# Kernel tuning notes

Measured on AMD Instinct MI355X. Metric: run time of the kernel, lower is better.

Reference implementation:

```python
import jax, jax.numpy as jnp
import numpy as np

DIM = 2048
NUM_HEADS = 16
NUM_KV_HEADS = 4
HEAD_DIM = DIM // NUM_HEADS  # 128
ROPE_BASE = 10000.0
TRAIN_SEQ_LEN = 1024
EPS = 1.1920929e-07  # torch.finfo(float32).eps, used by F.rms_norm default


def _rope_tables(seq_len, dtype=jnp.float32):
    rd = HEAD_DIM  # rope_dims defaults to full head_dim
    if seq_len > TRAIN_SEQ_LEN:
        s = seq_len / TRAIN_SEQ_LEN
        base = ROPE_BASE * s ** (rd / (rd - 2))
    else:
        base = ROPE_BASE
    inv_freq = 1.0 / base ** (jnp.arange(0, rd, 2, dtype=jnp.float32) / rd)
    t = jnp.arange(seq_len, dtype=jnp.float32)
    freqs = jnp.outer(t, inv_freq)  # [S, rd//2]
    cos = jnp.cos(freqs)[None, :, None, :].astype(dtype)  # [1,S,1,rd//2]
    sin = jnp.sin(freqs)[None, :, None, :].astype(dtype)
    return cos, sin


def _rms_norm(x):
    var = jnp.mean(jnp.square(x), axis=-1, keepdims=True)
    return x * jax.lax.rsqrt(var + EPS)


def _apply_rotary(x, cos, sin):
    h = x.shape[-1] // 2
    x1, x2 = x[..., :h], x[..., h:]
    return jnp.concatenate((x1 * cos + x2 * sin, -x1 * sin + x2 * cos), axis=-1)


def setup_inputs() -> dict:
    key = jax.random.key(0)
    ks = jax.random.split(key, 6)
    B, S = 2, 2048
    kv_dim = NUM_KV_HEADS * HEAD_DIM
    x = jax.random.normal(ks[0], (B, S, DIM), dtype=jnp.float32)
    Wq = jax.random.normal(ks[1], (DIM, DIM), dtype=jnp.float32) * 0.02
    Wk = jax.random.normal(ks[2], (kv_dim, DIM), dtype=jnp.float32) * 0.02
    Wv = jax.random.normal(ks[3], (kv_dim, DIM), dtype=jnp.float32) * 0.02
    Wo = jax.random.normal(ks[4], (DIM, DIM), dtype=jnp.float32) * 0.02
    q_gain = jnp.full((NUM_HEADS,), 1.0, dtype=jnp.float32)
    return {"x": x, "Wq": Wq, "Wk": Wk, "Wv": Wv, "Wo": Wo, "q_gain": q_gain}


def reference(x, Wq, Wk, Wv, Wo, q_gain):
    B, S, D = x.shape
    H, Hkv, Dh = NUM_HEADS, NUM_KV_HEADS, HEAD_DIM
    # QKV projections (CastedLinear, no bias)
    q = (x @ Wq.T).reshape(B, S, H, Dh)
    k = (x @ Wk.T).reshape(B, S, Hkv, Dh)
    v = (x @ Wv.T).reshape(B, S, Hkv, Dh)
    # RMSNorm over head_dim (no learned weight)
    q = _rms_norm(q)
    k = _rms_norm(k)
    # RoPE (full head_dim, NTK-scaled since S > train_seq_len)
    cos, sin = _rope_tables(S, q.dtype)
    q = _apply_rotary(q, cos, sin)
    k = _apply_rotary(k, cos, sin)
    # per-head gain on q
    q = q * q_gain.astype(q.dtype)[None, None, :, None]
    # GQA: repeat_interleave kv heads
    reps = H // Hkv
    k = jnp.repeat(k, reps, axis=2)  # [B,S,H,Dh]
    v = jnp.repeat(v, reps, axis=2)
    # causal attention
    scale = 1.0 / jnp.sqrt(jnp.asarray(Dh, dtype=q.dtype))
    scores = jnp.einsum('bqhd,bkhd->bhqk', q, k) * scale  # [B,H,S,S]
    causal = jnp.tril(jnp.ones((S, S), dtype=bool))
    scores = jnp.where(causal[None, None], scores, jnp.finfo(scores.dtype).min)
    attn = jax.nn.softmax(scores, axis=-1)
    y = jnp.einsum('bhqk,bkhd->bqhd', attn, v)  # [B,S,H,Dh]
    return y.reshape(B, S, D) @ Wo.T
```

## Files before the change

kernel.cpp:

```cpp
#include <hip/hip_runtime.h>

#define DIMSZ 2048
#define NHEAD 16
#define NKV 4
#define HD 128
#define QKVD 3072
#define SEQ 2048
#define NTOK 4096

typedef __attribute__((ext_vector_type(8))) short short8;
typedef __attribute__((ext_vector_type(4))) float f32x4;
typedef unsigned short u16;

__device__ __forceinline__ u16 f2bf(float x) {
  union { float f; unsigned u; } v; v.f = x;
  unsigned r = v.u + 0x7fffu + ((v.u >> 16) & 1u);
  return (u16)(r >> 16);
}
__device__ __forceinline__ unsigned pack_bf2(float a, float b) {
  unsigned ua = __float_as_uint(a) + 0x8000u;
  unsigned ub = __float_as_uint(b) + 0x8000u;
  return __builtin_amdgcn_perm(ub, ua, 0x07060302);
}

__device__ __forceinline__ void gl_lds16(const void* g, void* l) {
  __builtin_amdgcn_global_load_lds(
      (const __attribute__((address_space(1))) void*)g,
      (__attribute__((address_space(3))) void*)l, 16, 0, 0);
}

template <int N> __device__ __forceinline__ void vmw() {
  asm volatile("s_waitcnt vmcnt(%0)" :: "n"(N) : "memory");
}
__device__ __forceinline__ void barsb() {
  __builtin_amdgcn_s_barrier();
  __builtin_amdgcn_sched_barrier(0);
}

__global__ __launch_bounds__(256)
void castAll(const float* __restrict__ x,  const float* __restrict__ Wq,
             const float* __restrict__ Wk, const float* __restrict__ Wv,
             const float* __restrict__ Wo, u16* __restrict__ xb,
             u16* __restrict__ Wqkvb, u16* __restrict__ Wob) {
  int i = blockIdx.x * 256 + threadIdx.x;
  int f = i * 4;
  const float* src; u16* dst; int off;
  if (f < 8388608)       { src = x;  dst = xb;    off = f; }
  else if (f < 12582912) { src = Wq; dst = Wqkvb; off = f - 8388608; }
  else if (f < 13631488) { src = Wk; dst = Wqkvb + 4194304; off = f - 12582912; }
  else if (f < 14680064) { src = Wv; dst = Wqkvb + 5242880; off = f - 13631488; }
  else                   { src = Wo; dst = Wob;   off = f - 14680064; }
  float4 v = *(const float4*)(src + off);
  ushort4 o;
  o.x = f2bf(v.x); o.y = f2bf(v.y); o.z = f2bf(v.z); o.w = f2bf(v.w);
  *(ushort4*)(dst + off) = o;
}

template <int NCT, bool F32OUT>
__global__ __launch_bounds__(512, 2)
void gemmX(const u16* __restrict__ A, const u16* __restrict__ W,
           void* __restrict__ Cv, int M, int N, int K) {
  __shared__ __align__(16) u16 As[2][256][64];
  __shared__ __align__(16) u16 Bs[2][NCT * 64][64];
  const int tid = threadIdx.x;
  const int l = tid & 63;
  const int w = tid >> 6;
  const int r = l & 15, q = l >> 4;
  const int wm = (w >> 2) * 128;
  const int wn = (w & 3) * (NCT * 16);

  const int nx  = N / (NCT * 64);
  const int cpx = gridDim.x >> 3;
  const int lid = (blockIdx.x & 7) * cpx + (blockIdx.x >> 3);
  const int m0 = (lid / nx) << 8;
  const int n0 = (lid % nx) * (NCT * 64);

  const int scol = ((l & 7) ^ (l >> 3)) << 3;
  const u16* Asrc = A + (long)(m0 + w * 8 + (l >> 3)) * K + scol;
  const u16* Bsrc = W + (long)(n0 + w * 8 + (l >> 3)) * K + scol;

  auto stA = [&](int d, int u, int kt) {
    gl_lds16(Asrc + (long)(u * 64) * K + kt * 64, &As[d][u * 64 + w * 8][0]);
  };
  auto stB = [&](int d, int u, int kt) {
    gl_lds16(Bsrc + (long)(u * 64) * K + kt * 64, &Bs[d][u * 64 + w * 8][0]);
  };
  auto lda = [&](int d, int rt, int ks) -> short8 {
    return *(const short8*)&As[d][wm + rt * 16 + r][(((ks << 2) | q) ^ (r & 7)) << 3];
  };
  auto ldb = [&](int d, int ct, int ks) -> short8 {
    return *(const short8*)&Bs[d][wn + ct * 16 + r][(((ks << 2) | q) ^ (r & 7)) << 3];
  };

  f32x4 acc[8][NCT] = {};
  short8 a[4][2];
  short8 bE[NCT][2];
  short8 bO[NCT][2];

#define QUAD(i_, AB, BR)                                                      \
  _Pragma("unroll") for (int ks_ = 0; ks_ < 2; ++ks_)                         \
  _Pragma("unroll") for (int c_ = 0; c_ < NCT; ++c_)                          \
    acc[(AB) + (i_)][c_] = __builtin_amdgcn_mfma_f32_16x16x32_bf16(           \
        a[i_][ks_], BR[c_][ks_], acc[(AB) + (i_)][c_], 0, 0, 0);

#pragma unroll
  for (int u = 0; u < NCT; ++u) stB(0, u, 0);
  stA(0, 0, 0); stA(0, 1, 0); stA(0, 2, 0); stA(0, 3, 0);
#pragma unroll
  for (int u = 0; u < NCT; ++u) stB(1, u, 1);
  stA(1, 0, 1); stA(1, 2, 1);
  vmw<NCT + 2>();
  barsb();
#pragma unroll
  for (int i = 0; i < 4; ++i) { a[i][0] = lda(0, i, 0); a[i][1] = lda(0, i, 1); }
#pragma unroll
  for (int c = 0; c < NCT; ++c) { bE[c][0] = ldb(0, c, 0); bE[c][1] = ldb(0, c, 1); }

  const int niter = K >> 7;
  for (int it = 0; it < niter; ++it) {
    const int kt1 = 2 * it + 1, kt2 = 2 * it + 2, kt3 = 2 * it + 3;
    const bool more = (it + 1 < niter);

    stA(1, 1, kt1); stA(1, 3, kt1);
    __builtin_amdgcn_s_setprio(1);
#pragma unroll
    for (int i_ = 0; i_ < 4; ++i_) {
      QUAD(i_, 0, bE);
      a[i_][0] = lda(0, 4 + i_, 0); a[i_][1] = lda(0, 4 + i_, 1);
    }
    __builtin_amdgcn_s_setprio(0);
    vmw<2>();
    barsb();

    if (more) {
#pragma unroll
      for (int u = 0; u < NCT; ++u) stB(0, u, kt2);
      stA(0, 0, kt2); stA(0, 2, kt2);
    }
    __builtin_amdgcn_s_setprio(1);
#pragma unroll
    for (int i_ = 0; i_ < 4; ++i_) {
      QUAD(i_, 4, bE);
      a[i_][0] = lda(1, i_, 0); a[i_][1] = lda(1, i_, 1);
      if (i_ == 0) {
#pragma unroll
        for (int c = 0; c < NCT; ++c) { bO[c][0] = ldb(1, c, 0); bO[c][1] = ldb(1, c, 1); }
      }
    }
    __builtin_amdgcn_s_setprio(0);
    if (more) vmw<NCT + 2>(); else vmw<0>();
    barsb();

    if (more) { stA(0, 1, kt2); stA(0, 3, kt2); }
    __builtin_amdgcn_s_setprio(1);
#pragma unroll
    for (int i_ = 0; i_ < 4; ++i_) {
      QUAD(i_, 0, bO);
      a[i_][0] = lda(1, 4 + i_, 0); a[i_][1] = lda(1, 4 + i_, 1);
    }
    __builtin_amdgcn_s_setprio(0);
    if (more) vmw<2>();
    barsb();

    if (more) {
#pragma unroll
      for (int u = 0; u < NCT; ++u) stB(1, u, kt3);
      stA(1, 0, kt3); stA(1, 2, kt3);
    }
    __builtin_amdgcn_s_setprio(1);
#pragma unroll
    for (int i_ = 0; i_ < 4; ++i_) {
      QUAD(i_, 4, bO);
      if (more) {
        a[i_][0] = lda(0, i_, 0); a[i_][1] = lda(0, i_, 1);
        if (i_ == 0) {
#pragma unroll
          for (int c = 0; c < NCT; ++c) { bE[c][0] = ldb(0, c, 0); bE[c][1] = ldb(0, c, 1); }
        }
      }
    }
    __builtin_amdgcn_s_setprio(0);
    if (more) vmw<NCT + 2>();
    barsb();
  }
#undef QUAD

#pragma unroll
  for (int i = 0; i < 8; ++i)
#pragma unroll
    for (int j = 0; j < NCT; ++j) {
      int row = m0 + wm + i * 16 + q * 4;
      int col = n0 + wn + j * 16 + r;
#pragma unroll
      for (int t = 0; t < 4; ++t) {
        if (F32OUT)
          ((float*)Cv)[(long)(row + t) * N + col] = acc[i][j][t];
        else
          ((u16*)Cv)[(long)(row + t) * N + col] = f2bf(acc[i][j][t]);
      }
    }
}

__global__ __launch_bounds__(256)
void prep(u16* __restrict__ qkv, const float* __restrict__ gain, float qsc,
          u16* __restrict__ vt) {
  if (blockIdx.x < 20480) {
    int gid  = blockIdx.x * 4 + (threadIdx.x >> 6);
    int lane = threadIdx.x & 63;
    int token = gid / 20;
    int idx   = gid % 20;
    int s     = token & (SEQ - 1);
    bool isq  = idx < 16;
    int off   = isq ? idx * HD : 2048 + (idx - 16) * HD;
    float psc = isq ? qsc * gain[idx & 15] : 1.0f;
    u16* p = qkv + (long)token * QKVD + off;
    union { unsigned u; float f; } c1, c2;
    c1.u = ((unsigned)p[lane]) << 16;
    c2.u = ((unsigned)p[lane + 64]) << 16;
    float x1 = c1.f, x2 = c2.f;
    float ss = x1 * x1 + x2 * x2;
#pragma unroll
    for (int d = 1; d < 64; d <<= 1) ss += __shfl_xor(ss, d);
    float rn = rsqrtf(ss * (1.0f / 128.0f) + 1.1920929e-07f) * psc;
    float lb = log2f(10000.0f) + 128.0f / 126.0f;
    float inv_freq = exp2f(-(float)lane * (lb * (1.0f / 64.0f)));
    float ang = (float)s * inv_freq;
    float sn, cs;
    sincosf(ang, &sn, &cs);
    p[lane]      = f2bf((x1 * cs + x2 * sn) * rn);
    p[lane + 64] = f2bf((-x1 * sn + x2 * cs) * rn);
  } else {
    __shared__ u16 T[128 * 72];
    int bid = blockIdx.x - 20480;
    const int k0 = (bid & 31) * 64, hkv = (bid >> 5) & 3, b = bid >> 7;
    const u16* vb = qkv + 2560;
    const int t = threadIdx.x;
    const int key = t & 63, dh0 = (t >> 6) * 32;
#pragma unroll
    for (int c = 0; c < 4; c++) {
      uint4 vv = *(const uint4*)&vb[(long)(b * SEQ + k0 + key) * QKVD + hkv * HD + dh0 + c * 8];
      u16 tmp[8];
      *(uint4*)tmp = vv;
#pragma unroll
      for (int e = 0; e < 8; e++) T[(dh0 + c * 8 + e) * 72 + key] = tmp[e];
    }
    __syncthreads();
    const int dh = t >> 1, half = t & 1;
#pragma unroll
    for (int c = 0; c < 4; c++) {
      uint4 ov = *(const uint4*)&T[dh * 72 + half * 32 + c * 8];
      *(uint4*)&vt[((long)(b * NKV + hkv) * HD + dh) * SEQ + k0 + half * 32 + c * 8] = ov;
    }
  }
}

__global__ __launch_bounds__(256, 4)
void fattn(const u16* __restrict__ qb, const u16* __restrict__ kb,
           const u16* __restrict__ vtg, u16* __restrict__ yb) {
  __shared__ u16 Ks[64 * 128];
  __shared__ u16 Vt[128 * 64];
  __shared__ u16 Ps[64 * 64];
  const int tid  = threadIdx.x;
  const int lane = tid & 63;
  const int w    = tid >> 6;
  const int r = lane & 15, q = lane >> 4;
  const int qt = 31 - (blockIdx.x >> 5);
  const int hb = blockIdx.x & 31;
  const int h  = hb >> 1;
  const int b  = hb & 1;
  const int q0 = qt * 64;
  const int hkv = h >> 2;

  long koff[4], voff[4];
  u16 *kdst[4], *vdst[4];
#pragma unroll
  for (int c = 0; c < 4; c++) {
    int gr = w * 16 + c * 4 + (lane >> 4);
    int s  = lane & 15;
    int kj = (s & 8) | ((s ^ gr) & 7);
    koff[c] = (long)gr * QKVD + hkv * HD + kj * 8;
    kdst[c] = Ks + (w * 16 + c * 4) * 128;
    int dh = (w * 4 + c) * 8 + (lane >> 3);
    int vs = lane & 7;
    int vj = (vs ^ dh) & 7;
    voff[c] = (long)dh * SEQ + vj * 8;
    vdst[c] = Vt + (w * 4 + c) * 8 * 64;
  }
  const u16* vbase = vtg + (long)(b * NKV + hkv) * HD * SEQ;

  short8 qf[4];
#pragma unroll
  for (int ks = 0; ks < 4; ks++)
    qf[ks] = *(const short8*)&qb[(long)(b * SEQ + q0 + w * 16 + r) * QKVD +
                                 h * HD + ks * 32 + q * 8];

  f32x4 oacc[8] = {};
  float l_i = 0.f;
  const int maskbase = q * 4 - w * 16 - r;
  const int psx = (r & 7) << 1;

  for (int k0 = 0; k0 <= q0; k0 += 64) {
    __syncthreads();
    const u16* kb_t = kb + (long)(b * SEQ + k0) * QKVD;
    const u16* vb_t = vbase + k0;
#pragma unroll
    for (int c = 0; c < 4; c++) {
      gl_lds16(kb_t + koff[c], kdst[c]);
      gl_lds16(vb_t + voff[c], vdst[c]);
    }
    __syncthreads();

    const bool maskit = (k0 == q0);

    f32x4 st[4] = {};
#pragma unroll
    for (int jt = 0; jt < 4; jt++)
#pragma unroll
      for (int ks = 0; ks < 4; ks++) {
        int row = jt * 16 + r;
        int j = ks * 4 + q;
        int p = (j & 8) | ((j ^ row) & 7);
        short8 kf = *(const short8*)&Ks[row * 128 + p * 8];
        st[jt] = __builtin_amdgcn_mfma_f32_16x16x32_bf16(kf, qf[ks], st[jt], 0, 0, 0);
      }

    if (maskit) {
#pragma unroll
      for (int jt = 0; jt < 4; jt++)
#pragma unroll
        for (int t = 0; t < 4; t++)
          if (jt * 16 + maskbase + t > 0) st[jt][t] = -3e38f;
    }

#pragma unroll
    for (int jt = 0; jt < 4; jt++) {
#pragma unroll
      for (int t = 0; t < 4; t++) {
        float p = exp2f(st[jt][t]);
        st[jt][t] = p;
      }
      l_i += (st[jt][0] + st[jt][1]) + (st[jt][2] + st[jt][3]);
      uint2 pk;
      pk.x = pack_bf2(st[jt][0], st[jt][1]);
      pk.y = pack_bf2(st[jt][2], st[jt][3]);
      *(uint2*)&Ps[(w * 16 + r) * 64 + ((jt * 4 + q) ^ psx) * 4] = pk;
    }
    asm volatile("s_waitcnt lgkmcnt(0)" ::: "memory");

#pragma unroll
    for (int ks = 0; ks < 2; ks++) {
      short8 pf = *(const short8*)&Ps[(w * 16 + r) * 64 + ((ks * 8 + q * 2) ^ psx) * 4];
#pragma unroll
      for (int n = 0; n < 8; n++) {
        int row = n * 16 + r;
        int j = ks * 4 + q;
        int p = (j ^ row) & 7;
        short8 vf = *(const short8*)&Vt[row * 64 + p * 8];
        oacc[n] = __builtin_amdgcn_mfma_f32_16x16x32_bf16(pf, vf, oacc[n], 0, 0, 0);
      }
    }
  }

  l_i += __shfl_xor(l_i, 16);
  l_i += __shfl_xor(l_i, 32);
  float lb4[4];
#pragma unroll
  for (int t = 0; t < 4; t++) lb4[t] = 1.0f / __shfl(l_i, q * 4 + t);
#pragma unroll
  for (int n = 0; n < 8; n++)
#pragma unroll
    for (int t = 0; t < 4; t++) {
      int row = q0 + w * 16 + q * 4 + t;
      int col = n * 16 + r;
      yb[(long)(b * SEQ + row) * DIMSZ + h * HD + col] = f2bf(oacc[n][t] * lb4[t]);
    }
}

extern "C" void kernel_launch(void* const* d_in, const int* in_sizes, int n_in,
                              void* d_out, int out_size, void* d_ws, size_t ws_size,
                              hipStream_t stream) {
  const float* x  = (const float*)d_in[0];
  const float* Wq = (const float*)d_in[1];
  const float* Wk = (const float*)d_in[2];
  const float* Wv = (const float*)d_in[3];
  const float* Wo = (const float*)d_in[4];
  const float* qg = (const float*)d_in[5];
  float* out = (float*)d_out;

  const long MB = 1024 * 1024;
  char* ws = (char*)d_ws;
  u16* xb    = (u16*)(ws + 0 * MB);
  u16* ybuf  = (u16*)(ws + 0 * MB);
  u16* Wqkvb = (u16*)(ws + 16 * MB);
  u16* Wob   = (u16*)(ws + 28 * MB);
  u16* qkv   = (u16*)(ws + 36 * MB);
  u16* vtg   = (u16*)(ws + 60 * MB);

  castAll<<<18432, 256, 0, stream>>>(x, Wq, Wk, Wv, Wo, xb, Wqkvb, Wob);

  gemmX<3, false><<<256, 512, 0, stream>>>(xb, Wqkvb, qkv, NTOK, QKVD, DIMSZ);

  const float qsc = 0.08838834764831845f * 1.44269504088896f;
  prep<<<20736, 256, 0, stream>>>(qkv, qg, qsc, vtg);

  fattn<<<1024, 256, 0, stream>>>(qkv, qkv + 2048, vtg, ybuf);

  gemmX<2, true><<<256, 512, 0, stream>>>(ybuf, Wob, out, NTOK, DIMSZ, DIMSZ);
}
```

Before: 296.6 us.

## Rewrite flash attention with 32x32 MFMA, 128-query tiles and register P

Restructures the attention kernel to use 32x32x16 bf16 MFMA with 128-row query tiles per block (32 rows per wave), halving the grid. The softmax probabilities stay in registers and are rearranged with v_permlane32_swap for the PV MFMA, so the Ps LDS buffer and its round trip go away. The block ordering is changed to pair long and short causal tiles, aimed at load balancing and at reusing each K/V tile across more queries. Occupancy drops to 2 blocks per CU, and there is one extra diagonal K tile iteration per block.

New measurement: 303.7 us. +2.4%, slower.

```diff
diff --git a/kernel.cpp b/kernel.cpp
--- a/kernel.cpp
+++ b/kernel.cpp
@@ -10,6 +10,7 @@
 
 typedef __attribute__((ext_vector_type(8))) short short8;
 typedef __attribute__((ext_vector_type(4))) float f32x4;
+typedef __attribute__((ext_vector_type(16))) float f32x16;
 typedef unsigned short u16;
 
 __device__ __forceinline__ u16 f2bf(float x) {
@@ -254,52 +255,66 @@
   }
 }
 
-__global__ __launch_bounds__(256, 4)
+__global__ __launch_bounds__(256, 2)
 void fattn(const u16* __restrict__ qb, const u16* __restrict__ kb,
            const u16* __restrict__ vtg, u16* __restrict__ yb) {
   __shared__ u16 Ks[64 * 128];
   __shared__ u16 Vt[128 * 64];
-  __shared__ u16 Ps[64 * 64];
-  const int tid  = threadIdx.x;
-  const int lane = tid & 63;
-  const int w    = tid >> 6;
-  const int r = lane & 15, q = lane >> 4;
-  const int qt = 31 - (blockIdx.x >> 5);
-  const int hb = blockIdx.x & 31;
-  const int h  = hb >> 1;
-  const int b  = hb & 1;
-  const int q0 = qt * 64;
+  const int tid = threadIdx.x;
+  const int l   = tid & 63;
+  const int w   = tid >> 6;
+  const int lh  = l >> 5;
+  const int l31 = l & 31;
+  const int bq  = blockIdx.x >> 5;
+  const int qt  = (blockIdx.x & 256) ? (bq - 8) : (15 - bq);
+  const int hb  = blockIdx.x & 31;
+  const int h   = hb >> 1;
+  const int b   = hb & 1;
+  const int q0  = qt * 128;
   const int hkv = h >> 2;
-
-  long koff[4], voff[4];
+  const int qrow = q0 + w * 32 + l31;
+
+  int koff[4], voff[4];
   u16 *kdst[4], *vdst[4];
 #pragma unroll
   for (int c = 0; c < 4; c++) {
-    int gr = w * 16 + c * 4 + (lane >> 4);
-    int s  = lane & 15;
-    int kj = (s & 8) | ((s ^ gr) & 7);
-    koff[c] = (long)gr * QKVD + hkv * HD + kj * 8;
+    int gr = w * 16 + c * 4 + (l >> 4);
+    int s  = l & 15;
+    int kj = s ^ (gr & 15);
+    koff[c] = gr * QKVD + hkv * HD + kj * 8;
     kdst[c] = Ks + (w * 16 + c * 4) * 128;
-    int dh = (w * 4 + c) * 8 + (lane >> 3);
-    int vs = lane & 7;
-    int vj = (vs ^ dh) & 7;
-    voff[c] = (long)dh * SEQ + vj * 8;
-    vdst[c] = Vt + (w * 4 + c) * 8 * 64;
+    int dh = w * 32 + c * 8 + (l >> 3);
+    int vs = l & 7;
+    int vj = vs ^ (dh & 7);
+    voff[c] = dh * SEQ + vj * 8;
+    vdst[c] = Vt + (w * 32 + c * 8) * 64;
   }
   const u16* vbase = vtg + (long)(b * NKV + hkv) * HD * SEQ;
 
-  short8 qf[4];
-#pragma unroll
-  for (int ks = 0; ks < 4; ks++)
-    qf[ks] = *(const short8*)&qb[(long)(b * SEQ + q0 + w * 16 + r) * QKVD +
-                                 h * HD + ks * 32 + q * 8];
-
-  f32x4 oacc[8] = {};
+  short8 qf[8];
+  {
+    const u16* qp = qb + (long)(b * SEQ + qrow) * QKVD + h * HD + lh * 8;
+#pragma unroll
+    for (int ks = 0; ks < 8; ks++)
+      qf[ks] = *(const short8*)(qp + ks * 16);
+  }
+
+  f32x16 oacc[4] = {};
   float l_i = 0.f;
-  const int maskbase = q * 4 - w * 16 - r;
-  const int psx = (r & 7) << 1;
-
-  for (int k0 = 0; k0 <= q0; k0 += 64) {
+
+  auto kfr = [&](int kt, int ks) -> short8 {
+    int row = kt * 32 + l31;
+    int p = (ks * 2 + lh) ^ (row & 15);
+    return *(const short8*)&Ks[row * 128 + p * 8];
+  };
+  auto vfr = [&](int dt, int kq) -> short8 {
+    int row = dt * 32 + l31;
+    int p = (kq * 2 + lh) ^ (row & 7);
+    return *(const short8*)&Vt[row * 64 + p * 8];
+  };
+
+  const int kend = q0 + 64;
+  for (int k0 = 0; k0 <= kend; k0 += 64) {
     __syncthreads();
     const u16* kb_t = kb + (long)(b * SEQ + k0) * QKVD;
     const u16* vb_t = vbase + k0;
@@ -310,70 +325,62 @@
     }
     __syncthreads();
 
-    const bool maskit = (k0 == q0);
-
-    f32x4 st[4] = {};
-#pragma unroll
-    for (int jt = 0; jt < 4; jt++)
-#pragma unroll
-      for (int ks = 0; ks < 4; ks++) {
-        int row = jt * 16 + r;
-        int j = ks * 4 + q;
-        int p = (j & 8) | ((j ^ row) & 7);
-        short8 kf = *(const short8*)&Ks[row * 128 + p * 8];
-        st[jt] = __builtin_amdgcn_mfma_f32_16x16x32_bf16(kf, qf[ks], st[jt], 0, 0, 0);
-      }
-
-    if (maskit) {
-#pragma unroll
-      for (int jt = 0; jt < 4; jt++)
-#pragma unroll
-        for (int t = 0; t < 4; t++)
-          if (jt * 16 + maskbase + t > 0) st[jt][t] = -3e38f;
-    }
-
-#pragma unroll
-    for (int jt = 0; jt < 4; jt++) {
-#pragma unroll
-      for (int t = 0; t < 4; t++) {
-        float p = exp2f(st[jt][t]);
-        st[jt][t] = p;
-      }
-      l_i += (st[jt][0] + st[jt][1]) + (st[jt][2] + st[jt][3]);
-      uint2 pk;
-      pk.x = pack_bf2(st[jt][0], st[jt][1]);
-      pk.y = pack_bf2(st[jt][2], st[jt][3]);
-      *(uint2*)&Ps[(w * 16 + r) * 64 + ((jt * 4 + q) ^ psx) * 4] = pk;
-    }
-    asm volatile("s_waitcnt lgkmcnt(0)" ::: "memory");
-
-#pragma unroll
-    for (int ks = 0; ks < 2; ks++) {
-      short8 pf = *(const short8*)&Ps[(w * 16 + r) * 64 + ((ks * 8 + q * 2) ^ psx) * 4];
-#pragma unroll
-      for (int n = 0; n < 8; n++) {
-        int row = n * 16 + r;
-        int j = ks * 4 + q;
-        int p = (j ^ row) & 7;
-        short8 vf = *(const short8*)&Vt[row * 64 + p * 8];
-        oacc[n] = __builtin_amdgcn_mfma_f32_16x16x32_bf16(pf, vf, oacc[n], 0, 0, 0);
-      }
-    }
-  }
-
-  l_i += __shfl_xor(l_i, 16);
+    const bool diag = (k0 >= q0);
+
+#pragma unroll
+    for (int kt = 0; kt < 2; ++kt) {
+      f32x16 st;
+#pragma unroll
+      for (int g = 0; g < 16; ++g) st[g] = 0.f;
+#pragma unroll
+      for (int ks = 0; ks < 8; ++ks)
+        st = __builtin_amdgcn_mfma_f32_32x32x16_bf16(kfr(kt, ks), qf[ks], st, 0, 0, 0);
+
+      if (diag) {
+#pragma unroll
+        for (int g = 0; g < 16; ++g) {
+          int key = k0 + kt * 32 + (g & 3) + 8 * (g >> 2) + 4 * lh;
+          if (key > qrow) st[g] = -3e38f;
+        }
+      }
+
+#pragma unroll
+      for (int g = 0; g < 16; ++g) {
+        float e = exp2f(st[g]);
+        st[g] = e;
+        l_i += e;
+      }
+
+      unsigned c8[8];
+#pragma unroll
+      for (int m = 0; m < 8; ++m) c8[m] = pack_bf2(st[2 * m], st[2 * m + 1]);
+      asm("v_permlane32_swap_b32 %0, %1" : "+v"(c8[0]), "+v"(c8[2]));
+      asm("v_permlane32_swap_b32 %0, %1" : "+v"(c8[1]), "+v"(c8[3]));
+      asm("v_permlane32_swap_b32 %0, %1" : "+v"(c8[4]), "+v"(c8[6]));
+      asm("v_permlane32_swap_b32 %0, %1" : "+v"(c8[5]), "+v"(c8[7]));
+      union { unsigned u[4]; short8 s; } pa0, pa1;
+      pa0.u[0] = c8[0]; pa0.u[1] = c8[1]; pa0.u[2] = c8[2]; pa0.u[3] = c8[3];
+      pa1.u[0] = c8[4]; pa1.u[1] = c8[5]; pa1.u[2] = c8[6]; pa1.u[3] = c8[7];
+
+#pragma unroll
+      for (int dt = 0; dt < 4; ++dt) {
+        oacc[dt] = __builtin_amdgcn_mfma_f32_32x32x16_bf16(pa0.s, vfr(dt, kt * 2 + 0), oacc[dt], 0, 0, 0);
+        oacc[dt] = __builtin_amdgcn_mfma_f32_32x32x16_bf16(pa1.s, vfr(dt, kt * 2 + 1), oacc[dt], 0, 0, 0);
+      }
+    }
+  }
+
   l_i += __shfl_xor(l_i, 32);
-  float lb4[4];
-#pragma unroll
-  for (int t = 0; t < 4; t++) lb4[t] = 1.0f / __shfl(l_i, q * 4 + t);
-#pragma unroll
-  for (int n = 0; n < 8; n++)
-#pragma unroll
-    for (int t = 0; t < 4; t++) {
-      int row = q0 + w * 16 + q * 4 + t;
-      int col = n * 16 + r;
-      yb[(long)(b * SEQ + row) * DIMSZ + h * HD + col] = f2bf(oacc[n][t] * lb4[t]);
-    }
+  float linv = 1.0f / l_i;
+#pragma unroll
+  for (int g = 0; g < 16; ++g) {
+    int qrl = (g & 3) + 8 * (g >> 2) + 4 * lh;
+    float lg = __shfl(linv, qrl);
+    long rowoff = (long)(b * SEQ + q0 + w * 32 + qrl) * DIMSZ + h * HD + l31;
+#pragma unroll
+    for (int dt = 0; dt < 4; ++dt)
+      yb[rowoff + dt * 32] = f2bf(oacc[dt][g] * lg);
+  }
 }
 
 extern "C" void kernel_launch(void* const* d_in, const int* in_sizes, int n_in,
@@ -403,7 +410,7 @@
   const float qsc = 0.08838834764831845f * 1.44269504088896f;
   prep<<<20736, 256, 0, stream>>>(qkv, qg, qsc, vtg);
 
-  fattn<<<1024, 256, 0, stream>>>(qkv, qkv + 2048, vtg, ybuf);
+  fattn<<<512, 256, 0, stream>>>(qkv, qkv + 2048, vtg, ybuf);
 
   gemmX<2, true><<<256, 512, 0, stream>>>(ybuf, Wob, out, NTOK, DIMSZ, DIMSZ);
 }
```
